# Kernel optimization log

Hardware: AMD Instinct MI355X
Metric: run time of the kernel (lower is better)

Reference implementation:

```python
import jax, jax.numpy as jnp
import numpy as np

NEG_SLOPE = 0.2
H = 2  # num_heads (hardcoded in the torch module)


def _gat_conv(x, W, al, ar, b, src, dst, n_nodes):
    """DGL GATConv: x [N,F] -> [N,H,D]."""
    D = al.shape[1]
    h = (x @ W).reshape(n_nodes, H, D)               # [N,H,D]
    el = jnp.einsum('nhd,hd->nh', h, al)              # [N,H]
    er = jnp.einsum('nhd,hd->nh', h, ar)              # [N,H]
    e = el[src] + er[dst]                             # [E,H]
    e = jnp.where(e >= 0, e, NEG_SLOPE * e)           # LeakyReLU
    # edge softmax over incoming edges of each dst (every node has a self loop)
    m = jax.ops.segment_max(e, dst, num_segments=n_nodes)      # [N,H]
    ex = jnp.exp(e - m[dst])                                    # [E,H]
    s = jax.ops.segment_sum(ex, dst, num_segments=n_nodes)     # [N,H]
    alpha = ex / s[dst]                                         # [E,H]
    msg = alpha[:, :, None] * h[src]                             # [E,H,D]
    out = jax.ops.segment_sum(msg, dst, num_segments=n_nodes)   # [N,H,D]
    return out + b.reshape(1, H, D)


def setup_inputs() -> dict:
    key = jax.random.key(0)
    ks = jax.random.split(key, 10)
    N, E, F_IN, HID, OUT = 100000, 1600000, 128, 64, 64
    sc = 0.05
    return {
        'x':   jax.random.normal(ks[0], (N, F_IN), jnp.float32),
        'src': jax.random.randint(ks[1], (E,), 0, N, jnp.int32),
        'dst': jax.random.randint(ks[2], (E,), 0, N, jnp.int32),
        'W1':  jax.random.normal(ks[3], (F_IN, H * HID), jnp.float32) * sc,
        'al1': jax.random.normal(ks[4], (H, HID), jnp.float32) * sc,
        'ar1': jax.random.normal(ks[5], (H, HID), jnp.float32) * sc,
        'b1':  jnp.zeros((H * HID,), jnp.float32),
        'W2':  jax.random.normal(ks[6], (H * HID, H * OUT), jnp.float32) * sc,
        'al2': jax.random.normal(ks[7], (H, OUT), jnp.float32) * sc,
        'ar2': jax.random.normal(ks[8], (H, OUT), jnp.float32) * sc,
        'b2':  jnp.zeros((H * OUT,), jnp.float32),
    }


def reference(x, src, dst, W1, al1, ar1, b1, W2, al2, ar2, b2):
    N = x.shape[0]
    # dgl.add_self_loop
    loop = jnp.arange(N, dtype=src.dtype)
    s = jnp.concatenate([src, loop])
    d = jnp.concatenate([dst, loop])
    h = _gat_conv(x, W1, al1, ar1, b1, s, d, N)       # [N,H,HID]
    h = jax.nn.relu(h).reshape(N, -1)                  # flatten heads
    out = _gat_conv(h, W2, al2, ar2, b2, s, d, N)      # [N,H,OUT]
    return out.reshape(N, -1)
```

## Files before the change

### kernel.cpp

```cpp
#include <hip/hip_runtime.h>
#include <hip/hip_fp16.h>


#define NEG_SLOPE 0.2f
#define BSHIFT 8
#define ETILE 4096

typedef _Float16 half8_t __attribute__((ext_vector_type(8)));
typedef float f32x4_t __attribute__((ext_vector_type(4)));
typedef unsigned long long u64;


__global__ __launch_bounds__(256) void k_prepcount(const float* __restrict__ W1,
                                                   const float* __restrict__ W2,
                                                   __half* __restrict__ wh1,
                                                   __half* __restrict__ wh2,
                                                   const int* __restrict__ dst, int E,
                                                   int nbuck, int* __restrict__ bcnt) {
    int b = blockIdx.x;
    int t = threadIdx.x;
    if (b < 16) {
        const float* W = (b < 8) ? W1 : W2;
        __half* Wh = (b < 8) ? wh1 : wh2;
        int q = (b & 7) * 256 + t;
        int r = q >> 4;
        int c = q & 15;
        int cl = c ^ (r & 7);
        float f[8];
        #pragma unroll
        for (int j = 0; j < 8; j++) f[j] = W[(size_t)(cl * 8 + j) * 128 + r];
        __half2 h0 = __floats2half2_rn(f[0], f[1]);
        __half2 h1 = __floats2half2_rn(f[2], f[3]);
        __half2 h2 = __floats2half2_rn(f[4], f[5]);
        __half2 h3 = __floats2half2_rn(f[6], f[7]);
        uint4 pk;
        pk.x = *(unsigned*)&h0;
        pk.y = *(unsigned*)&h1;
        pk.z = *(unsigned*)&h2;
        pk.w = *(unsigned*)&h3;
        *(uint4*)((char*)Wh + (size_t)q * 16) = pk;
    } else {
        __shared__ int cnt[512];
        for (int i = t; i < nbuck; i += 256) cnt[i] = 0;
        __syncthreads();
        int e0 = (b - 16) * ETILE;
        #pragma unroll
        for (int j = 0; j < ETILE / 256; j++) {
            int e = e0 + j * 256 + t;
            if (e < E) atomicAdd(&cnt[dst[e] >> BSHIFT], 1);
        }
        __syncthreads();
        for (int i = t; i < nbuck; i += 256) {
            int c = cnt[i];
            if (c > 0) atomicAdd(&bcnt[i], c);
        }
    }
}


__global__ __launch_bounds__(256) void k_bscan(const int* __restrict__ bcnt, int nbuck,
                                               int* __restrict__ bbase,
                                               int* __restrict__ bcursor,
                                               int* __restrict__ rowStart, int N, int E) {
    __shared__ int sa[512], sb[512];
    int t = threadIdx.x;
    sa[t] = (t < nbuck) ? bcnt[t] : 0;
    sa[t + 256] = (t + 256 < nbuck) ? bcnt[t + 256] : 0;
    __syncthreads();
    int* a = sa;
    int* b = sb;
    for (int off = 1; off < 512; off <<= 1) {
        b[t] = a[t] + ((t >= off) ? a[t - off] : 0);
        int i = t + 256;
        b[i] = a[i] + ((i >= off) ? a[i - off] : 0);
        __syncthreads();
        int* tmp = a; a = b; b = tmp;
    }
    #pragma unroll
    for (int k = 0; k < 2; k++) {
        int i = t + k * 256;
        if (i <= nbuck) {
            int e_ = (i == 0) ? 0 : a[i - 1];
            bbase[i] = e_;
            if (i < nbuck) bcursor[i] = e_;
        }
    }
    if (t == 0) rowStart[N] = E;
}


__global__ __launch_bounds__(256) void k_build(const int* __restrict__ ebuf,
                                               const int* __restrict__ bbase,
                                               int* __restrict__ rowStart,
                                               int* __restrict__ csr, int N) {
    __shared__ int dcnt[256];
    __shared__ int sa[256], sb[256];
    __shared__ int cur[256];
    int b = blockIdx.x;
    int t = threadIdx.x;
    int lo = bbase[b], hi = bbase[b + 1];
    int n0 = b << BSHIFT;
    dcnt[t] = 0;
    __syncthreads();
    for (int p = lo + t; p < hi; p += 256)
        atomicAdd(&dcnt[((unsigned)ebuf[p]) >> 17], 1);
    __syncthreads();
    sa[t] = dcnt[t];
    __syncthreads();
    int* a = sa;
    int* bq = sb;
    for (int off = 1; off < 256; off <<= 1) {
        bq[t] = a[t] + ((t >= off) ? a[t - off] : 0);
        __syncthreads();
        int* tmp = a; a = bq; bq = tmp;
    }
    int excl = (t == 0) ? 0 : a[t - 1];
    int pos0 = lo + excl;
    if (n0 + t < N) rowStart[n0 + t] = pos0;
    cur[t] = pos0;
    __syncthreads();
    for (int p = lo + t; p < hi; p += 256) {
        int v = ebuf[p];
        int pos = atomicAdd(&cur[((unsigned)v) >> 17], 1);
        csr[pos] = v & 0x1FFFF;
    }
}


__device__ __forceinline__ void g2l16(const void* g, void* l) {
    __builtin_amdgcn_global_load_lds((const __attribute__((address_space(1))) void*)g,
                                     (__attribute__((address_space(3))) void*)l, 16, 0, 0);
}

template <bool FP16IN, bool BUCKET>
__global__ __launch_bounds__(256, 3) void k_gemm_fused(const void* __restrict__ Ain,
                                                       const __half* __restrict__ WhT,
                                                       __half* __restrict__ hb,
                                                       const float* __restrict__ al,
                                                       const float* __restrict__ ar,
                                                       float* __restrict__ el,
                                                       float* __restrict__ er, int M,
                                                       const int* __restrict__ srcE,
                                                       const int* __restrict__ dstE, int E,
                                                       int nbuck, int* __restrict__ bcursor,
                                                       int* __restrict__ ebuf,
                                                       int bucketBlocks) {
    __shared__ __half xs[64 * 128];
    __shared__ __half ws[128 * 128];
    int t = threadIdx.x;

    if (BUCKET && (int)blockIdx.x < bucketBlocks) {
        int* cnt = (int*)xs;
        int* base = cnt + 512;
        for (int b = t; b < nbuck; b += 256) cnt[b] = 0;
        __syncthreads();
        int e0 = (int)blockIdx.x * ETILE;
        int dv[ETILE / 256], sv[ETILE / 256];
        #pragma unroll
        for (int j = 0; j < ETILE / 256; j++) {
            int e = e0 + j * 256 + t;
            dv[j] = -1;
            if (e < E) {
                dv[j] = dstE[e];
                sv[j] = srcE[e];
                atomicAdd(&cnt[dv[j] >> BSHIFT], 1);
            }
        }
        __syncthreads();
        for (int b = t; b < nbuck; b += 256) {
            int c = cnt[b];
            base[b] = (c > 0) ? atomicAdd(&bcursor[b], c) : 0;
        }
        __syncthreads();
        for (int b = t; b < nbuck; b += 256) cnt[b] = 0;
        __syncthreads();
        #pragma unroll
        for (int j = 0; j < ETILE / 256; j++) {
            if (dv[j] >= 0) {
                int bk = dv[j] >> BSHIFT;
                int r = atomicAdd(&cnt[bk], 1);
                ebuf[base[bk] + r] = sv[j] | ((dv[j] & ((1 << BSHIFT) - 1)) << 17);
            }
        }
        return;
    }

    int row0 = (BUCKET ? ((int)blockIdx.x - bucketBlocks) : (int)blockIdx.x) * 64;
    for (int j = 0; j < 8; j++) {
        int c16 = t + j * 256;
        g2l16((const char*)WhT + (size_t)c16 * 16, (char*)ws + (size_t)c16 * 16);
    }
    if (FP16IN) {
        const char* Ah = (const char*)Ain;
        for (int j = 0; j < 4; j++) {
            int c16 = t + j * 256;
            g2l16(Ah + (size_t)row0 * 256 + (size_t)c16 * 16, (char*)xs + (size_t)c16 * 16);
        }
    } else {
        const float* A = (const float*)Ain;
        for (int j = 0; j < 8; j++) {
            int f4 = t + j * 256;
            int r = f4 >> 5;
            int gr = row0 + r;
            if (gr >= M) gr = M - 1;
            float4 v = ((const float4*)(A + (size_t)gr * 128))[f4 & 31];
            __half2 h0 = __floats2half2_rn(v.x, v.y);
            __half2 h1 = __floats2half2_rn(v.z, v.w);
            uint2 pk;
            pk.x = *(unsigned*)&h0;
            pk.y = *(unsigned*)&h1;
            int h8 = f4 & 31;
            int c = h8 >> 1, hh = h8 & 1;
            int addr8 = r * 32 + (c ^ (r & 7)) * 2 + hh;
            *(uint2*)((char*)xs + (size_t)addr8 * 8) = pk;
        }
    }
    __syncthreads();

    int wid = t >> 6, lane = t & 63;
    int l15 = lane & 15;
    int g = lane >> 4;
    int mrow = wid * 16 + l15;

    half8_t xf[4];
    #pragma unroll
    for (int ks = 0; ks < 4; ks++) {
        int c = ks * 4 + g;
        xf[ks] = *(const half8_t*)((const char*)xs + mrow * 256 + (size_t)(c ^ (mrow & 7)) * 16);
    }

    f32x4_t acc[8];
    #pragma unroll
    for (int i = 0; i < 8; i++) acc[i] = (f32x4_t){0.f, 0.f, 0.f, 0.f};

    #pragma unroll
    for (int nt = 0; nt < 8; nt++) {
        int nrow = nt * 16 + l15;
        #pragma unroll
        for (int ks = 0; ks < 4; ks++) {
            int c = ks * 4 + g;
            half8_t wf = *(const half8_t*)((const char*)ws + nrow * 256 + (size_t)(c ^ (nrow & 7)) * 16);
            acc[nt] = __builtin_amdgcn_mfma_f32_16x16x32_f16(wf, xf[ks], acc[nt], 0, 0, 0);
        }
    }

    int m = row0 + wid * 16 + l15;
    bool valid = m < M;
    float plh0 = 0.f, prh0 = 0.f, plh1 = 0.f, prh1 = 0.f;
    #pragma unroll
    for (int nt = 0; nt < 8; nt++) {
        int col0 = nt * 16 + g * 4;
        if (valid) {
            __half2 p0 = __floats2half2_rn(acc[nt][0], acc[nt][1]);
            __half2 p1 = __floats2half2_rn(acc[nt][2], acc[nt][3]);
            uint2 pk;
            pk.x = *(unsigned*)&p0;
            pk.y = *(unsigned*)&p1;
            *(uint2*)(hb + (size_t)m * 128 + col0) = pk;
        }
        float4 alv = *(const float4*)(al + col0);
        float4 arv = *(const float4*)(ar + col0);
        float pl = acc[nt][0] * alv.x + acc[nt][1] * alv.y + acc[nt][2] * alv.z + acc[nt][3] * alv.w;
        float pr = acc[nt][0] * arv.x + acc[nt][1] * arv.y + acc[nt][2] * arv.z + acc[nt][3] * arv.w;
        if (nt < 4) { plh0 += pl; prh0 += pr; }
        else       { plh1 += pl; prh1 += pr; }
    }
    plh0 += __shfl_xor(plh0, 16); plh0 += __shfl_xor(plh0, 32);
    plh1 += __shfl_xor(plh1, 16); plh1 += __shfl_xor(plh1, 32);
    prh0 += __shfl_xor(prh0, 16); prh0 += __shfl_xor(prh0, 32);
    prh1 += __shfl_xor(prh1, 16); prh1 += __shfl_xor(prh1, 32);
    if (lane < 16 && valid) {
        el[m * 2 + 0] = plh0;
        el[m * 2 + 1] = plh1;
        er[m * 2 + 0] = prh0;
        er[m * 2 + 1] = prh1;
    }
}


__device__ __forceinline__ float h2f(__half h) { return __half2float(h); }

template <bool RELU, bool FP16OUT>
__global__ __launch_bounds__(256) void k_agg(const __half* __restrict__ hb,
                                             const float* __restrict__ el,
                                             const float* __restrict__ er,
                                             const int* __restrict__ rowStart,
                                             const int* __restrict__ csr,
                                             const float* __restrict__ bias,
                                             void* __restrict__ outv, int N) {
    __shared__ u64 albuf[4][4][65];
    int wid = threadIdx.x >> 6;
    int lane = threadIdx.x & 63;
    int q = lane >> 4;
    int l = lane & 15;
    int n = (blockIdx.x * 4 + wid) * 4 + q;
    bool active = n < N;

    int rs = 0, deg = 0;
    float2 erv = make_float2(0.f, 0.f);
    if (active) {
        rs = rowStart[n];
        deg = rowStart[n + 1] - rs;
        erv = ((const float2*)er)[n];
    }

    float s0 = 0.f, s1 = 0.f;
    if (active) {
        for (int i = l; i <= deg; i += 16) {
            int s = (i == deg) ? n : csr[rs + i];
            float2 ev = ((const float2*)el)[s];
            float e0 = ev.x + erv.x;
            e0 = (e0 >= 0.f) ? e0 : NEG_SLOPE * e0;
            float e1 = ev.y + erv.y;
            e1 = (e1 >= 0.f) ? e1 : NEG_SLOPE * e1;
            float ex0 = __expf(e0);
            float ex1 = __expf(e1);
            s0 += ex0;
            s1 += ex1;
            if (i < 64) {
                __half2 eh = __floats2half2_rn(ex0, ex1);
                albuf[wid][q][i] = ((u64)(*(unsigned*)&eh) << 32) | (u64)(unsigned)s;
            }
        }
    }
    #pragma unroll
    for (int mk = 8; mk >= 1; mk >>= 1) {
        s0 += __shfl_xor(s0, mk);
        s1 += __shfl_xor(s1, mk);
    }
    bool hi = l >= 8;
    float invh = hi ? (1.0f / s1) : (1.0f / s0);

    float a0 = 0.f, a1 = 0.f, a2 = 0.f, a3 = 0.f;
    float a4 = 0.f, a5 = 0.f, a6 = 0.f, a7 = 0.f;
    if (active) {
        int cnt = deg + 1;
        int jmax = (cnt < 64) ? cnt : 64;
        int j = 0;
        for (; j + 4 <= jmax; j += 4) {
            u64 r0 = albuf[wid][q][j + 0];
            u64 r1 = albuf[wid][q][j + 1];
            u64 r2 = albuf[wid][q][j + 2];
            u64 r3 = albuf[wid][q][j + 3];
            uint4 v0 = ((const uint4*)(hb + (size_t)(unsigned)r0 * 128))[l];
            uint4 v1 = ((const uint4*)(hb + (size_t)(unsigned)r1 * 128))[l];
            uint4 v2 = ((const uint4*)(hb + (size_t)(unsigned)r2 * 128))[l];
            uint4 v3 = ((const uint4*)(hb + (size_t)(unsigned)r3 * 128))[l];
            #pragma unroll
            for (int kk = 0; kk < 4; kk++) {
                u64 rec = (kk == 0) ? r0 : (kk == 1) ? r1 : (kk == 2) ? r2 : r3;
                uint4 hv = (kk == 0) ? v0 : (kk == 1) ? v1 : (kk == 2) ? v2 : v3;
                unsigned eb = (unsigned)(rec >> 32);
                __half hx;
                *(unsigned short*)&hx = (unsigned short)(hi ? (eb >> 16) : (eb & 0xffff));
                float a = h2f(hx);
                __half2 p0 = *(__half2*)&hv.x;
                __half2 p1 = *(__half2*)&hv.y;
                __half2 p2 = *(__half2*)&hv.z;
                __half2 p3 = *(__half2*)&hv.w;
                a0 += a * h2f(p0.x);  a1 += a * h2f(p0.y);
                a2 += a * h2f(p1.x);  a3 += a * h2f(p1.y);
                a4 += a * h2f(p2.x);  a5 += a * h2f(p2.y);
                a6 += a * h2f(p3.x);  a7 += a * h2f(p3.y);
            }
        }
        for (; j < jmax; ++j) {
            u64 rec = albuf[wid][q][j];
            unsigned eb = (unsigned)(rec >> 32);
            __half hx;
            *(unsigned short*)&hx = (unsigned short)(hi ? (eb >> 16) : (eb & 0xffff));
            float a = h2f(hx);
            uint4 hv = ((const uint4*)(hb + (size_t)(unsigned)rec * 128))[l];
            __half2 p0 = *(__half2*)&hv.x;
            __half2 p1 = *(__half2*)&hv.y;
            __half2 p2 = *(__half2*)&hv.z;
            __half2 p3 = *(__half2*)&hv.w;
            a0 += a * h2f(p0.x);  a1 += a * h2f(p0.y);
            a2 += a * h2f(p1.x);  a3 += a * h2f(p1.y);
            a4 += a * h2f(p2.x);  a5 += a * h2f(p2.y);
            a6 += a * h2f(p3.x);  a7 += a * h2f(p3.y);
        }
        for (int jj = 64; jj < cnt; ++jj) {
            int s = (jj == deg) ? n : csr[rs + jj];
            float2 ev = ((const float2*)el)[s];
            float e = hi ? (ev.y + erv.y) : (ev.x + erv.x);
            e = (e >= 0.f) ? e : NEG_SLOPE * e;
            float a = __expf(e);
            uint4 hv = ((const uint4*)(hb + (size_t)s * 128))[l];
            __half2 p0 = *(__half2*)&hv.x;
            __half2 p1 = *(__half2*)&hv.y;
            __half2 p2 = *(__half2*)&hv.z;
            __half2 p3 = *(__half2*)&hv.w;
            a0 += a * h2f(p0.x);  a1 += a * h2f(p0.y);
            a2 += a * h2f(p1.x);  a3 += a * h2f(p1.y);
            a4 += a * h2f(p2.x);  a5 += a * h2f(p2.y);
            a6 += a * h2f(p3.x);  a7 += a * h2f(p3.y);
        }

        const float4* bp = (const float4*)(bias + l * 8);
        float4 b0 = bp[0], b1 = bp[1];
        a0 = a0 * invh + b0.x;  a1 = a1 * invh + b0.y;
        a2 = a2 * invh + b0.z;  a3 = a3 * invh + b0.w;
        a4 = a4 * invh + b1.x;  a5 = a5 * invh + b1.y;
        a6 = a6 * invh + b1.z;  a7 = a7 * invh + b1.w;
        if (RELU) {
            a0 = fmaxf(a0, 0.f); a1 = fmaxf(a1, 0.f); a2 = fmaxf(a2, 0.f); a3 = fmaxf(a3, 0.f);
            a4 = fmaxf(a4, 0.f); a5 = fmaxf(a5, 0.f); a6 = fmaxf(a6, 0.f); a7 = fmaxf(a7, 0.f);
        }
        if (FP16OUT) {
            __half2 q0 = __floats2half2_rn(a0, a1);
            __half2 q1 = __floats2half2_rn(a2, a3);
            __half2 q2 = __floats2half2_rn(a4, a5);
            __half2 q3 = __floats2half2_rn(a6, a7);
            uint4 opk;
            opk.x = *(unsigned*)&q0;
            opk.y = *(unsigned*)&q1;
            opk.z = *(unsigned*)&q2;
            opk.w = *(unsigned*)&q3;
            ((uint4*)((__half*)outv + (size_t)n * 128))[l ^ (n & 7)] = opk;
        } else {
            float* op = (float*)outv + (size_t)n * 128 + l * 8;
            ((float4*)op)[0] = make_float4(a0, a1, a2, a3);
            ((float4*)op)[1] = make_float4(a4, a5, a6, a7);
        }
    }
}


static inline size_t align_up(size_t v, size_t a) { return (v + a - 1) & ~(a - 1); }

extern "C" void kernel_launch(void* const* d_in, const int* in_sizes, int n_in,
                              void* d_out, int out_size, void* d_ws, size_t ws_size,
                              hipStream_t stream) {
    const float* x   = (const float*)d_in[0];
    const int*   src = (const int*)d_in[1];
    const int*   dst = (const int*)d_in[2];
    const float* W1  = (const float*)d_in[3];
    const float* al1 = (const float*)d_in[4];
    const float* ar1 = (const float*)d_in[5];
    const float* b1  = (const float*)d_in[6];
    const float* W2  = (const float*)d_in[7];
    const float* al2 = (const float*)d_in[8];
    const float* ar2 = (const float*)d_in[9];
    const float* b2  = (const float*)d_in[10];
    float* out = (float*)d_out;

    const int N = in_sizes[0] / 128;
    const int E = in_sizes[1];
    const int NBUCK = (N + 255) >> 8;

    char* ws = (char*)d_ws;
    size_t off = 0;
    __half* bufBh = (__half*)(ws + off); off = align_up(off + (size_t)N * 128 * 2, 256);
    __half* hb    = (__half*)(ws + off); off = align_up(off + (size_t)N * 128 * 2 + 16384, 256);
    float* el   = (float*)(ws + off); off = align_up(off + (size_t)N * 2 * 4, 256);
    float* er   = (float*)(ws + off); off = align_up(off + (size_t)N * 2 * 4, 256);
    int* rowStart = (int*)(ws + off); off = align_up(off + (size_t)(N + 1) * 4, 256);
    int* csr      = (int*)(ws + off); off = align_up(off + (size_t)E * 4, 256);
    int* ebuf     = (int*)(ws + off); off = align_up(off + (size_t)E * 4, 256);
    int* bcnt     = (int*)(ws + off); off = align_up(off + (size_t)NBUCK * 4, 256);
    int* bbase    = (int*)(ws + off); off = align_up(off + (size_t)(NBUCK + 1) * 4, 256);
    int* bcursor  = (int*)(ws + off); off = align_up(off + (size_t)NBUCK * 4, 256);
    __half* wh1   = (__half*)(ws + off); off = align_up(off + (size_t)16384 * 2, 256);
    __half* wh2   = (__half*)(ws + off); off = align_up(off + (size_t)16384 * 2, 256);

    const int etile_grid = (E + ETILE - 1) / ETILE;
    const int gemm_grid = (N + 63) / 64;
    const int agg_grid = (N + 15) / 16;

    hipMemsetAsync(bcnt, 0, (size_t)NBUCK * 4, stream);
    k_prepcount<<<16 + etile_grid, 256, 0, stream>>>(W1, W2, wh1, wh2, dst, E, NBUCK, bcnt);
    k_bscan<<<1, 256, 0, stream>>>(bcnt, NBUCK, bbase, bcursor, rowStart, N, E);

    k_gemm_fused<false, true><<<etile_grid + gemm_grid, 256, 0, stream>>>(
        x, wh1, hb, al1, ar1, el, er, N, src, dst, E, NBUCK, bcursor, ebuf, etile_grid);

    k_build<<<NBUCK, 256, 0, stream>>>(ebuf, bbase, rowStart, csr, N);

    k_agg<true, true><<<agg_grid, 256, 0, stream>>>(hb, el, er, rowStart, csr, b1, bufBh, N);

    k_gemm_fused<true, false><<<gemm_grid, 256, 0, stream>>>(
        bufBh, wh2, hb, al2, ar2, el, er, N, nullptr, nullptr, 0, 0, nullptr, nullptr, 0);

    k_agg<false, false><<<agg_grid, 256, 0, stream>>>(hb, el, er, rowStart, csr, b2, out, N);
}
```

Measured before the change: 225.8 us.

## Co-schedule CSR build with half of layer-1 GEMM to remove standalone build kernel

The layer-1 GEMM is split into two halves. The first half runs alongside the edge bucketing blocks, and the second half runs alongside the per-bucket CSR build blocks, which were folded into the fused kernel. This removes a separate k_build launch and lets the GEMM work overlap with the irregular build work. The cost is two launches that each carry only half the GEMM, plus an extra template branch in the fused kernel.

After: 223.5 us. Within noise of the previous version (-1.0%).

```diff
diff --git a/kernel.cpp b/kernel.cpp
--- a/kernel.cpp
+++ b/kernel.cpp
@@ -89,50 +89,12 @@
 }
 
 
-__global__ __launch_bounds__(256) void k_build(const int* __restrict__ ebuf,
-                                               const int* __restrict__ bbase,
-                                               int* __restrict__ rowStart,
-                                               int* __restrict__ csr, int N) {
-    __shared__ int dcnt[256];
-    __shared__ int sa[256], sb[256];
-    __shared__ int cur[256];
-    int b = blockIdx.x;
-    int t = threadIdx.x;
-    int lo = bbase[b], hi = bbase[b + 1];
-    int n0 = b << BSHIFT;
-    dcnt[t] = 0;
-    __syncthreads();
-    for (int p = lo + t; p < hi; p += 256)
-        atomicAdd(&dcnt[((unsigned)ebuf[p]) >> 17], 1);
-    __syncthreads();
-    sa[t] = dcnt[t];
-    __syncthreads();
-    int* a = sa;
-    int* bq = sb;
-    for (int off = 1; off < 256; off <<= 1) {
-        bq[t] = a[t] + ((t >= off) ? a[t - off] : 0);
-        __syncthreads();
-        int* tmp = a; a = bq; bq = tmp;
-    }
-    int excl = (t == 0) ? 0 : a[t - 1];
-    int pos0 = lo + excl;
-    if (n0 + t < N) rowStart[n0 + t] = pos0;
-    cur[t] = pos0;
-    __syncthreads();
-    for (int p = lo + t; p < hi; p += 256) {
-        int v = ebuf[p];
-        int pos = atomicAdd(&cur[((unsigned)v) >> 17], 1);
-        csr[pos] = v & 0x1FFFF;
-    }
-}
-
-
 __device__ __forceinline__ void g2l16(const void* g, void* l) {
     __builtin_amdgcn_global_load_lds((const __attribute__((address_space(1))) void*)g,
                                      (__attribute__((address_space(3))) void*)l, 16, 0, 0);
 }
 
-template <bool FP16IN, bool BUCKET>
+template <bool FP16IN, int JOB>
 __global__ __launch_bounds__(256, 3) void k_gemm_fused(const void* __restrict__ Ain,
                                                        const __half* __restrict__ WhT,
                                                        __half* __restrict__ hb,
@@ -144,12 +106,15 @@
                                                        const int* __restrict__ dstE, int E,
                                                        int nbuck, int* __restrict__ bcursor,
                                                        int* __restrict__ ebuf,
-                                                       int bucketBlocks) {
+                                                       const int* __restrict__ bbase,
+                                                       int* __restrict__ rowStart,
+                                                       int* __restrict__ csr,
+                                                       int sideBlocks, int rowBase) {
     __shared__ __half xs[64 * 128];
     __shared__ __half ws[128 * 128];
     int t = threadIdx.x;
 
-    if (BUCKET && (int)blockIdx.x < bucketBlocks) {
+    if (JOB == 1 && (int)blockIdx.x < sideBlocks) {
         int* cnt = (int*)xs;
         int* base = cnt + 512;
         for (int b = t; b < nbuck; b += 256) cnt[b] = 0;
@@ -185,7 +150,43 @@
         return;
     }
 
-    int row0 = (BUCKET ? ((int)blockIdx.x - bucketBlocks) : (int)blockIdx.x) * 64;
+    if (JOB == 2 && (int)blockIdx.x < sideBlocks) {
+        int* dcnt = (int*)xs;
+        int* sa = dcnt + 256;
+        int* sb = sa + 256;
+        int* cur = sb + 256;
+        int b = blockIdx.x;
+        int lo = bbase[b], hi2 = bbase[b + 1];
+        int n0 = b << BSHIFT;
+        dcnt[t] = 0;
+        __syncthreads();
+        for (int p = lo + t; p < hi2; p += 256)
+            atomicAdd(&dcnt[((unsigned)ebuf[p]) >> 17], 1);
+        __syncthreads();
+        sa[t] = dcnt[t];
+        __syncthreads();
+        int* a = sa;
+        int* bq = sb;
+        for (int off2 = 1; off2 < 256; off2 <<= 1) {
+            bq[t] = a[t] + ((t >= off2) ? a[t - off2] : 0);
+            __syncthreads();
+            int* tmp = a; a = bq; bq = tmp;
+        }
+        int excl = (t == 0) ? 0 : a[t - 1];
+        int pos0 = lo + excl;
+        if (n0 + t < M) rowStart[n0 + t] = pos0;
+        cur[t] = pos0;
+        __syncthreads();
+        for (int p = lo + t; p < hi2; p += 256) {
+            int v = ebuf[p];
+            int pos = atomicAdd(&cur[((unsigned)v) >> 17], 1);
+            csr[pos] = v & 0x1FFFF;
+        }
+        return;
+    }
+
+    int row0 = ((JOB ? ((int)blockIdx.x - sideBlocks) : (int)blockIdx.x) + rowBase) * 64;
+
     for (int j = 0; j < 8; j++) {
         int c16 = t + j * 256;
         g2l16((const char*)WhT + (size_t)c16 * 16, (char*)ws + (size_t)c16 * 16);
@@ -244,7 +245,7 @@
         }
     }
 
-    int m = row0 + wid * 16 + l15;
+    int m = row0 + mrow;
     bool valid = m < M;
     float plh0 = 0.f, prh0 = 0.f, plh1 = 0.f, prh1 = 0.f;
     #pragma unroll
@@ -466,21 +467,27 @@
 
     const int etile_grid = (E + ETILE - 1) / ETILE;
     const int gemm_grid = (N + 63) / 64;
+    const int gA = (gemm_grid + 1) / 2;
+    const int gB = gemm_grid - gA;
     const int agg_grid = (N + 15) / 16;
 
     hipMemsetAsync(bcnt, 0, (size_t)NBUCK * 4, stream);
     k_prepcount<<<16 + etile_grid, 256, 0, stream>>>(W1, W2, wh1, wh2, dst, E, NBUCK, bcnt);
     k_bscan<<<1, 256, 0, stream>>>(bcnt, NBUCK, bbase, bcursor, rowStart, N, E);
 
-    k_gemm_fused<false, true><<<etile_grid + gemm_grid, 256, 0, stream>>>(
-        x, wh1, hb, al1, ar1, el, er, N, src, dst, E, NBUCK, bcursor, ebuf, etile_grid);
-
-    k_build<<<NBUCK, 256, 0, stream>>>(ebuf, bbase, rowStart, csr, N);
+    k_gemm_fused<false, 1><<<etile_grid + gA, 256, 0, stream>>>(
+        x, wh1, hb, al1, ar1, el, er, N, src, dst, E, NBUCK, bcursor, ebuf,
+        nullptr, nullptr, nullptr, etile_grid, 0);
+
+    k_gemm_fused<false, 2><<<NBUCK + gB, 256, 0, stream>>>(
+        x, wh1, hb, al1, ar1, el, er, N, nullptr, nullptr, 0, NBUCK, nullptr, ebuf,
+        bbase, rowStart, csr, NBUCK, gA);
 
     k_agg<true, true><<<agg_grid, 256, 0, stream>>>(hb, el, er, rowStart, csr, b1, bufBh, N);
 
-    k_gemm_fused<true, false><<<gemm_grid, 256, 0, stream>>>(
-        bufBh, wh2, hb, al2, ar2, el, er, N, nullptr, nullptr, 0, 0, nullptr, nullptr, 0);
+    k_gemm_fused<true, 0><<<gemm_grid, 256, 0, stream>>>(
+        bufBh, wh2, hb, al2, ar2, el, er, N, nullptr, nullptr, 0, 0, nullptr, nullptr,
+        nullptr, nullptr, nullptr, 0, 0);
 
     k_agg<false, false><<<agg_grid, 256, 0, stream>>>(hb, el, er, rowStart, csr, b2, out, N);
 }
```
